# Kernel optimization log

Measured on AMD Instinct MI355X. Metric: run time of the kernel, lower is better.

## Reference

```python
import jax, jax.numpy as jnp
import numpy as np

BATCH = 16384
NUM_IN = 4096
NUM_OUT = 1024
NNZ = 262144
BN_EPS = 1e-3  # keras BatchNormalization default epsilon


def setup_inputs() -> dict:
    key = jax.random.key(0)
    ks = jax.random.split(key, 6)
    x = jax.random.normal(ks[0], (BATCH, NUM_IN), dtype=jnp.float32)
    sp_values = jax.random.normal(ks[1], (NNZ,), dtype=jnp.float32)
    gamma = jnp.ones((NUM_IN,), dtype=jnp.float32)
    beta = jnp.zeros((NUM_IN,), dtype=jnp.float32)
    moving_mean = jax.random.normal(ks[2], (NUM_IN,), dtype=jnp.float32)
    # positive moving variance in [0.5, 1.5)
    moving_var = jax.random.uniform(ks[3], (NUM_IN,), dtype=jnp.float32, minval=0.5, maxval=1.5)
    sp_rows = jax.random.randint(ks[4], (NNZ,), 0, NUM_IN, dtype=jnp.int32)
    sp_cols = jax.random.randint(ks[5], (NNZ,), 0, NUM_OUT, dtype=jnp.int32)
    return {
        "x": x,
        "sp_values": sp_values,
        "gamma": gamma,
        "beta": beta,
        "moving_mean": moving_mean,
        "moving_var": moving_var,
        "sp_rows": sp_rows,
        "sp_cols": sp_cols,
    }


def reference(x, sp_values, gamma, beta, moving_mean, moving_var, sp_rows, sp_cols):
    # BatchNorm (inference mode, moving statistics), fused elementwise
    h = (x - moving_mean) * (gamma * jax.lax.rsqrt(moving_var + BN_EPS)) + beta
    # Scatter the fixed-index sparse weights into a small dense [NUM_IN, NUM_OUT]
    # matrix (16 MB), then a single dense GEMM — honors SparseTensor semantics
    # (duplicate indices accumulate) while staying GEMM-efficient.
    W = jnp.zeros((NUM_IN, NUM_OUT), dtype=x.dtype).at[sp_rows, sp_cols].add(sp_values)
    return h @ W  # [BATCH, NUM_OUT]
```

## Files before the change

### kernel.cpp

```cpp
#include <hip/hip_runtime.h>
#include <hip/hip_bf16.h>

#define BATCH   16384
#define NUM_IN  4096
#define NUM_OUT 1024
#define NNZ     262144
#define BN_EPS  1e-3f

typedef __attribute__((ext_vector_type(8))) short   short8;
typedef __attribute__((ext_vector_type(4))) float   f32x4;
typedef __attribute__((ext_vector_type(4))) unsigned int u32x4;

typedef __attribute__((address_space(3))) void        lds_void_t;
typedef const __attribute__((address_space(1))) void  g_void_t;

__device__ inline unsigned short f2bf(float f) {
    unsigned int u = __builtin_bit_cast(unsigned int, f);
    u += 0x7fffu + ((u >> 16) & 1u);
    return (unsigned short)(u >> 16);
}

__global__ void k_zero(f32x4* __restrict__ p) {
    p[(size_t)blockIdx.x * 256 + threadIdx.x] = f32x4{0.f, 0.f, 0.f, 0.f};
}

__global__ void k_scatter(const float* __restrict__ v, const int* __restrict__ r,
                          const int* __restrict__ c, float* __restrict__ wtf) {
    int i = blockIdx.x * 256 + threadIdx.x;
    atomicAdd(&wtf[(size_t)c[i] * NUM_IN + r[i]], v[i]);
}

__global__ void k_wprep(const float* __restrict__ wtf, const float* __restrict__ gamma,
                        const float* __restrict__ beta, const float* __restrict__ mean,
                        const float* __restrict__ var, unsigned short* __restrict__ wtb,
                        float* __restrict__ bias) {
    const int n = blockIdx.x;
    const int t = threadIdx.x;
    float acc = 0.f;
    for (int k = t; k < NUM_IN; k += 256) {
        float w = wtf[(size_t)n * NUM_IN + k];
        float s = gamma[k] * rsqrtf(var[k] + BN_EPS);
        wtb[(size_t)n * NUM_IN + k] = f2bf(w * s);
        acc += (beta[k] - mean[k] * s) * w;
    }
    #pragma unroll
    for (int o = 32; o; o >>= 1) acc += __shfl_down(acc, o, 64);
    __shared__ float red[4];
    if ((t & 63) == 0) red[t >> 6] = acc;
    __syncthreads();
    if (t == 0) bias[n] = red[0] + red[1] + red[2] + red[3];
}

#define BM 256
#define BN 256
#define BK 32
#define KTILES (NUM_IN / BK)
#define ABYTES 32768
#define BBYTES 16384
#define PBUF   49152

__global__ __launch_bounds__(512, 2) void k_gemm(const float* __restrict__ x,
                                                 const unsigned short* __restrict__ wt,
                                                 const float* __restrict__ bias,
                                                 float* __restrict__ out) {
    __shared__ __align__(128) char lds[3 * PBUF];

    const int bid = blockIdx.x;
    const int swz = (bid & 7) * 32 + (bid >> 3);
    const int m0 = (swz >> 2) * BM;
    const int n0 = (swz & 3) * BN;

    const int t    = threadIdx.x;
    const int lane = t & 63;
    const int wid  = t >> 6;
    const int wm   = wid >> 1;
    const int wn   = wid & 1;

    const char* xb = (const char*)x;
    const char* wb = (const char*)wt;

    const int a_r0 = t >> 3, a_c = (t & 7) * 16;
    const int b_r0 = t >> 2, b_c = (t & 3) * 16;

    auto stage = [&](int kt, int buf) {
        char* base = lds + buf * PBUF;
        #pragma unroll
        for (int q = 0; q < 4; ++q) {
            int row = q * 64 + a_r0;
            size_t src = (size_t)(m0 + row) * (NUM_IN * 4) + kt * (BK * 4)
                       + (a_c ^ ((row & 7) << 4));
            __builtin_amdgcn_global_load_lds((g_void_t*)(xb + src),
                (lds_void_t*)(base + q * 8192 + t * 16), 16, 0, 0);
        }
        #pragma unroll
        for (int q = 0; q < 2; ++q) {
            int row = q * 128 + b_r0;
            size_t src = (size_t)(n0 + row) * (NUM_IN * 2) + kt * (BK * 2)
                       + (b_c ^ (((row >> 1) & 3) << 4));
            __builtin_amdgcn_global_load_lds((g_void_t*)(wb + src),
                (lds_void_t*)(base + ABYTES + q * 8192 + t * 16), 16, 0, 0);
        }
    };

    f32x4 acc[4][8] = {};

    const int a_row0 = wm * 64 + (lane & 15);
    const int a_kb   = (lane >> 4) * 32;
    const int b_row0 = wn * 128 + (lane & 15);
    const int b_kb   = (lane >> 4) * 16;

    auto compute = [&](int buf) {
        const char* A = lds + buf * PBUF;
        const char* B = A + ABYTES;
        short8 bfr[8];
        #pragma unroll
        for (int j = 0; j < 8; ++j) {
            int row = b_row0 + j * 16;
            bfr[j] = *(const short8*)(B + row * 64 + (b_kb ^ (((row >> 1) & 3) << 4)));
        }
        short8 af[4];
        #pragma unroll
        for (int m = 0; m < 4; ++m) {
            int row = a_row0 + m * 16;
            int s = (row & 7) << 4;
            f32x4 lo = *(const f32x4*)(A + row * 128 + (a_kb ^ s));
            f32x4 hi = *(const f32x4*)(A + row * 128 + ((a_kb + 16) ^ s));
            const unsigned int* f0 = (const unsigned int*)&lo;
            const unsigned int* f1 = (const unsigned int*)&hi;
            u32x4 p;
            p[0] = __builtin_amdgcn_perm(f0[1], f0[0], 0x07060302u);
            p[1] = __builtin_amdgcn_perm(f0[3], f0[2], 0x07060302u);
            p[2] = __builtin_amdgcn_perm(f1[1], f1[0], 0x07060302u);
            p[3] = __builtin_amdgcn_perm(f1[3], f1[2], 0x07060302u);
            af[m] = __builtin_bit_cast(short8, p);
        }
        __builtin_amdgcn_s_setprio(1);
        #pragma unroll
        for (int m = 0; m < 4; ++m)
            #pragma unroll
            for (int j = 0; j < 8; ++j)
                acc[m][j] = __builtin_amdgcn_mfma_f32_16x16x32_bf16(af[m], bfr[j],
                                                                    acc[m][j], 0, 0, 0);
        __builtin_amdgcn_s_setprio(0);
    };

    stage(0, 0);
    stage(1, 1);
    asm volatile("s_waitcnt vmcnt(6)" ::: "memory");
    __builtin_amdgcn_s_barrier();
    __builtin_amdgcn_sched_barrier(0);

    int cur = 0, sb = 2;
    for (int kt = 0; kt < KTILES - 2; ++kt) {
        stage(kt + 2, sb);
        compute(cur);
        asm volatile("s_waitcnt vmcnt(6)" ::: "memory");
        __builtin_amdgcn_s_barrier();
        __builtin_amdgcn_sched_barrier(0);
        cur = (cur == 2) ? 0 : cur + 1;
        sb  = (sb  == 2) ? 0 : sb  + 1;
    }
    compute(cur);
    cur = (cur == 2) ? 0 : cur + 1;
    asm volatile("s_waitcnt vmcnt(0)" ::: "memory");
    __builtin_amdgcn_s_barrier();
    __builtin_amdgcn_sched_barrier(0);
    compute(cur);

    float bj[8];
    #pragma unroll
    for (int j = 0; j < 8; ++j) bj[j] = bias[n0 + wn * 128 + j * 16 + (lane & 15)];
    const int mb = m0 + wm * 64 + (lane >> 4) * 4;
    const int nb = n0 + wn * 128 + (lane & 15);
    #pragma unroll
    for (int m = 0; m < 4; ++m)
        #pragma unroll
        for (int j = 0; j < 8; ++j)
            #pragma unroll
            for (int r = 0; r < 4; ++r)
                out[(size_t)(mb + m * 16 + r) * NUM_OUT + (nb + j * 16)] =
                    acc[m][j][r] + bj[j];
}

extern "C" void kernel_launch(void* const* d_in, const int* in_sizes, int n_in,
                              void* d_out, int out_size, void* d_ws, size_t ws_size,
                              hipStream_t stream) {
    const float* x     = (const float*)d_in[0];
    const float* spv   = (const float*)d_in[1];
    const float* gamma = (const float*)d_in[2];
    const float* beta  = (const float*)d_in[3];
    const float* mean  = (const float*)d_in[4];
    const float* var   = (const float*)d_in[5];
    const int*   rows  = (const int*)d_in[6];
    const int*   cols  = (const int*)d_in[7];
    float* out = (float*)d_out;

    float* wtf = (float*)d_out;
    unsigned short* wtb = (unsigned short*)d_ws;
    float* bias = (float*)((char*)d_ws + (size_t)NUM_IN * NUM_OUT * sizeof(unsigned short));

    hipLaunchKernelGGL(k_zero, dim3((NUM_IN * NUM_OUT / 4) / 256), dim3(256), 0, stream,
                       (f32x4*)wtf);
    hipLaunchKernelGGL(k_scatter, dim3(NNZ / 256), dim3(256), 0, stream,
                       spv, rows, cols, wtf);
    hipLaunchKernelGGL(k_wprep, dim3(NUM_OUT), dim3(256), 0, stream,
                       wtf, gamma, beta, mean, var, wtb, bias);
    hipLaunchKernelGGL(k_gemm, dim3((BATCH / BM) * (NUM_OUT / BN)), dim3(512), 0, stream,
                       x, wtb, bias, out);
}
```

Before: 191.1 us.

## Convert A tile to bf16 once in LDS and switch to 32x32x16 MFMA

Result: slower. 238.6 us (+24.9%).

```diff
diff --git a/kernel.cpp b/kernel.cpp
--- a/kernel.cpp
+++ b/kernel.cpp
@@ -7,9 +7,10 @@
 #define NNZ     262144
 #define BN_EPS  1e-3f
 
-typedef __attribute__((ext_vector_type(8))) short   short8;
-typedef __attribute__((ext_vector_type(4))) float   f32x4;
-typedef __attribute__((ext_vector_type(4))) unsigned int u32x4;
+typedef __attribute__((ext_vector_type(8)))  short short8;
+typedef __attribute__((ext_vector_type(4)))  float f32x4;
+typedef __attribute__((ext_vector_type(16))) float f32x16;
+typedef __attribute__((ext_vector_type(4)))  unsigned int u32x4;
 
 typedef __attribute__((address_space(3))) void        lds_void_t;
 typedef const __attribute__((address_space(1))) void  g_void_t;
@@ -54,16 +55,15 @@
 #define BM 256
 #define BN 256
 #define BK 32
-#define KTILES (NUM_IN / BK)
-#define ABYTES 32768
-#define BBYTES 16384
-#define PBUF   49152
+#define NT (NUM_IN / BK)
+#define SLOT 32768
+#define B_OFF 16384
 
 __global__ __launch_bounds__(512, 2) void k_gemm(const float* __restrict__ x,
                                                  const unsigned short* __restrict__ wt,
                                                  const float* __restrict__ bias,
                                                  float* __restrict__ out) {
-    __shared__ __align__(128) char lds[3 * PBUF];
+    __shared__ __align__(128) char lds[4 * SLOT];
 
     const int bid = blockIdx.x;
     const int swz = (bid & 7) * 32 + (bid >> 3);
@@ -73,113 +73,143 @@
     const int t    = threadIdx.x;
     const int lane = t & 63;
     const int wid  = t >> 6;
-    const int wm   = wid >> 1;
-    const int wn   = wid & 1;
+    const int wm   = wid >> 2;
+    const int wn   = wid & 3;
 
     const char* xb = (const char*)x;
     const char* wb = (const char*)wt;
 
-    const int a_r0 = t >> 3, a_c = (t & 7) * 16;
-    const int b_r0 = t >> 2, b_c = (t & 3) * 16;
-
-    auto stage = [&](int kt, int buf) {
-        char* base = lds + buf * PBUF;
-        #pragma unroll
-        for (int q = 0; q < 4; ++q) {
-            int row = q * 64 + a_r0;
-            size_t src = (size_t)(m0 + row) * (NUM_IN * 4) + kt * (BK * 4)
-                       + (a_c ^ ((row & 7) << 4));
-            __builtin_amdgcn_global_load_lds((g_void_t*)(xb + src),
-                (lds_void_t*)(base + q * 8192 + t * 16), 16, 0, 0);
-        }
-        #pragma unroll
-        for (int q = 0; q < 2; ++q) {
-            int row = q * 128 + b_r0;
-            size_t src = (size_t)(n0 + row) * (NUM_IN * 2) + kt * (BK * 2)
-                       + (b_c ^ (((row >> 1) & 3) << 4));
+    const int s_ar  = t >> 1;
+    const int s_ah  = t & 1;
+    const int a_swz = ((s_ar >> 1) & 3) << 4;
+    const int s_bc  = t >> 2;
+    const int s_bk  = (t & 3) * 16;
+
+    f32x4 rA[2][4];
+
+    auto stageB = [&](int kt, int slot) {
+        #pragma unroll
+        for (int i = 0; i < 2; ++i) {
+            int c = i * 128 + s_bc;
+            size_t src = (size_t)(n0 + c) * (NUM_IN * 2) + kt * (BK * 2)
+                       + (s_bk ^ (((c >> 1) & 3) << 4));
             __builtin_amdgcn_global_load_lds((g_void_t*)(wb + src),
-                (lds_void_t*)(base + ABYTES + q * 8192 + t * 16), 16, 0, 0);
-        }
-    };
-
-    f32x4 acc[4][8] = {};
-
-    const int a_row0 = wm * 64 + (lane & 15);
-    const int a_kb   = (lane >> 4) * 32;
-    const int b_row0 = wn * 128 + (lane & 15);
-    const int b_kb   = (lane >> 4) * 16;
-
-    auto compute = [&](int buf) {
-        const char* A = lds + buf * PBUF;
-        const char* B = A + ABYTES;
-        short8 bfr[8];
-        #pragma unroll
-        for (int j = 0; j < 8; ++j) {
-            int row = b_row0 + j * 16;
-            bfr[j] = *(const short8*)(B + row * 64 + (b_kb ^ (((row >> 1) & 3) << 4)));
-        }
-        short8 af[4];
+                (lds_void_t*)(lds + slot * SLOT + B_OFF + i * 8192 + t * 16), 16, 0, 0);
+        }
+    };
+    auto loadA = [&](int kt, int rs) {
+        size_t src = (size_t)(m0 + s_ar) * (NUM_IN * 4) + kt * (BK * 4) + s_ah * 64;
+        #pragma unroll
+        for (int j = 0; j < 4; ++j)
+            rA[rs][j] = *(const f32x4*)(xb + src + j * 16);
+    };
+    auto writeA = [&](int slot, int rs) {
+        const unsigned int* f = (const unsigned int*)&rA[rs][0];
+        u32x4 p0, p1;
+        p0[0] = __builtin_amdgcn_perm(f[1],  f[0],  0x07060302u);
+        p0[1] = __builtin_amdgcn_perm(f[3],  f[2],  0x07060302u);
+        p0[2] = __builtin_amdgcn_perm(f[5],  f[4],  0x07060302u);
+        p0[3] = __builtin_amdgcn_perm(f[7],  f[6],  0x07060302u);
+        p1[0] = __builtin_amdgcn_perm(f[9],  f[8],  0x07060302u);
+        p1[1] = __builtin_amdgcn_perm(f[11], f[10], 0x07060302u);
+        p1[2] = __builtin_amdgcn_perm(f[13], f[12], 0x07060302u);
+        p1[3] = __builtin_amdgcn_perm(f[15], f[14], 0x07060302u);
+        char* dst = lds + slot * SLOT + s_ar * 64;
+        *(u32x4*)(dst + ((s_ah * 32 +  0) ^ a_swz)) = p0;
+        *(u32x4*)(dst + ((s_ah * 32 + 16) ^ a_swz)) = p1;
+    };
+
+    const int fa_row = wm * 128 + (lane & 31);
+    const int fb_col = wn * 64 + (lane & 31);
+    const int f_kb   = (lane >> 5) * 16;
+
+    short8 afr[4], bfr[2];
+    auto readFrags = [&](int slot, int q) {
+        const char* A = lds + slot * SLOT;
+        const char* B = A + B_OFF;
         #pragma unroll
         for (int m = 0; m < 4; ++m) {
-            int row = a_row0 + m * 16;
-            int s = (row & 7) << 4;
-            f32x4 lo = *(const f32x4*)(A + row * 128 + (a_kb ^ s));
-            f32x4 hi = *(const f32x4*)(A + row * 128 + ((a_kb + 16) ^ s));
-            const unsigned int* f0 = (const unsigned int*)&lo;
-            const unsigned int* f1 = (const unsigned int*)&hi;
-            u32x4 p;
-            p[0] = __builtin_amdgcn_perm(f0[1], f0[0], 0x07060302u);
-            p[1] = __builtin_amdgcn_perm(f0[3], f0[2], 0x07060302u);
-            p[2] = __builtin_amdgcn_perm(f1[1], f1[0], 0x07060302u);
-            p[3] = __builtin_amdgcn_perm(f1[3], f1[2], 0x07060302u);
-            af[m] = __builtin_bit_cast(short8, p);
-        }
+            int row = fa_row + m * 32;
+            afr[m] = *(const short8*)(A + row * 64
+                       + ((q * 32 + f_kb) ^ (((row >> 1) & 3) << 4)));
+        }
+        #pragma unroll
+        for (int n = 0; n < 2; ++n) {
+            int col = fb_col + n * 32;
+            bfr[n] = *(const short8*)(B + col * 64
+                       + ((q * 32 + f_kb) ^ (((col >> 1) & 3) << 4)));
+        }
+    };
+
+    f32x16 acc[4][2] = {};
+    auto domfma = [&]() {
         __builtin_amdgcn_s_setprio(1);
         #pragma unroll
         for (int m = 0; m < 4; ++m)
             #pragma unroll
-            for (int j = 0; j < 8; ++j)
-                acc[m][j] = __builtin_amdgcn_mfma_f32_16x16x32_bf16(af[m], bfr[j],
-                                                                    acc[m][j], 0, 0, 0);
+            for (int n = 0; n < 2; ++n)
+                acc[m][n] = __builtin_amdgcn_mfma_f32_32x32x16_bf16(
+                    afr[m], bfr[n], acc[m][n], 0, 0, 0);
         __builtin_amdgcn_s_setprio(0);
     };
 
-    stage(0, 0);
-    stage(1, 1);
+    auto body = [&](int kt, int rs, bool doStage, bool doConv, bool vm0) {
+        const int cs = kt & 3;
+        if (doStage) {
+            stageB(kt + 2, (kt + 2) & 3);
+            loadA(kt + 2, rs);
+            __builtin_amdgcn_sched_barrier(0);
+        }
+        readFrags(cs, 0);
+        asm volatile("s_waitcnt lgkmcnt(0)" ::: "memory");
+        __builtin_amdgcn_sched_barrier(0);
+        domfma();
+        __builtin_amdgcn_s_barrier();
+        readFrags(cs, 1);
+        __builtin_amdgcn_sched_barrier(0);
+        if (doConv) {
+            if (vm0) asm volatile("s_waitcnt vmcnt(0)" ::: "memory");
+            else     asm volatile("s_waitcnt vmcnt(6)" ::: "memory");
+            writeA((kt + 1) & 3, rs ^ 1);
+            asm volatile("s_waitcnt lgkmcnt(2)" ::: "memory");
+        } else {
+            asm volatile("s_waitcnt lgkmcnt(0)" ::: "memory");
+        }
+        __builtin_amdgcn_sched_barrier(0);
+        domfma();
+        asm volatile("s_waitcnt lgkmcnt(0)" ::: "memory");
+        __builtin_amdgcn_s_barrier();
+    };
+
+    stageB(0, 0); loadA(0, 0);
+    stageB(1, 1); loadA(1, 1);
     asm volatile("s_waitcnt vmcnt(6)" ::: "memory");
+    writeA(0, 0);
+    asm volatile("s_waitcnt lgkmcnt(0)" ::: "memory");
     __builtin_amdgcn_s_barrier();
-    __builtin_amdgcn_sched_barrier(0);
-
-    int cur = 0, sb = 2;
-    for (int kt = 0; kt < KTILES - 2; ++kt) {
-        stage(kt + 2, sb);
-        compute(cur);
-        asm volatile("s_waitcnt vmcnt(6)" ::: "memory");
-        __builtin_amdgcn_s_barrier();
-        __builtin_amdgcn_sched_barrier(0);
-        cur = (cur == 2) ? 0 : cur + 1;
-        sb  = (sb  == 2) ? 0 : sb  + 1;
+
+    #pragma unroll 1
+    for (int kt = 0; kt < NT - 2; kt += 2) {
+        body(kt,     0, true, true, false);
+        body(kt + 1, 1, true, true, false);
     }
-    compute(cur);
-    cur = (cur == 2) ? 0 : cur + 1;
-    asm volatile("s_waitcnt vmcnt(0)" ::: "memory");
-    __builtin_amdgcn_s_barrier();
-    __builtin_amdgcn_sched_barrier(0);
-    compute(cur);
-
-    float bj[8];
+    body(NT - 2, 0, false, true, true);
+    body(NT - 1, 1, false, false, false);
+
+    float bj[2];
     #pragma unroll
-    for (int j = 0; j < 8; ++j) bj[j] = bias[n0 + wn * 128 + j * 16 + (lane & 15)];
-    const int mb = m0 + wm * 64 + (lane >> 4) * 4;
-    const int nb = n0 + wn * 128 + (lane & 15);
+    for (int n = 0; n < 2; ++n) bj[n] = bias[n0 + wn * 64 + n * 32 + (lane & 31)];
+    const int rbase = m0 + wm * 128 + 4 * (lane >> 5);
+    const int cbase = n0 + wn * 64 + (lane & 31);
     #pragma unroll
     for (int m = 0; m < 4; ++m)
         #pragma unroll
-        for (int j = 0; j < 8; ++j)
+        for (int n = 0; n < 2; ++n)
             #pragma unroll
-            for (int r = 0; r < 4; ++r)
-                out[(size_t)(mb + m * 16 + r) * NUM_OUT + (nb + j * 16)] =
-                    acc[m][j][r] + bj[j];
+            for (int r = 0; r < 16; ++r) {
+                int row = rbase + m * 32 + (r & 3) + 8 * (r >> 2);
+                out[(size_t)row * NUM_OUT + cbase + n * 32] = acc[m][n][r] + bj[n];
+            }
 }
 
 extern "C" void kernel_launch(void* const* d_in, const int* in_sizes, int n_in,
```

## Split GEMM K-step into two phases interleaving LDS reads, staging and MFMA

Applied to the files above, without the earlier changes.

Measured after the change: 206.3 us. 1.08x slower.

```diff
diff --git a/kernel.cpp b/kernel.cpp
--- a/kernel.cpp
+++ b/kernel.cpp
@@ -7,9 +7,9 @@
 #define NNZ     262144
 #define BN_EPS  1e-3f
 
-typedef __attribute__((ext_vector_type(8))) short   short8;
-typedef __attribute__((ext_vector_type(4))) float   f32x4;
-typedef __attribute__((ext_vector_type(4))) unsigned int u32x4;
+typedef __attribute__((ext_vector_type(8)))  short short8;
+typedef __attribute__((ext_vector_type(4)))  float f32x4;
+typedef __attribute__((ext_vector_type(4)))  unsigned int u32x4;
 
 typedef __attribute__((address_space(3))) void        lds_void_t;
 typedef const __attribute__((address_space(1))) void  g_void_t;
@@ -54,16 +54,16 @@
 #define BM 256
 #define BN 256
 #define BK 32
-#define KTILES (NUM_IN / BK)
-#define ABYTES 32768
-#define BBYTES 16384
-#define PBUF   49152
+#define NT (NUM_IN / BK)
+#define ASLOT 32768
+#define BSLOT 16384
+#define PSLOT 49152
 
 __global__ __launch_bounds__(512, 2) void k_gemm(const float* __restrict__ x,
                                                  const unsigned short* __restrict__ wt,
                                                  const float* __restrict__ bias,
                                                  float* __restrict__ out) {
-    __shared__ __align__(128) char lds[3 * PBUF];
+    __shared__ __align__(128) char lds[3 * PSLOT];
 
     const int bid = blockIdx.x;
     const int swz = (bid & 7) * 32 + (bid >> 3);
@@ -73,60 +73,61 @@
     const int t    = threadIdx.x;
     const int lane = t & 63;
     const int wid  = t >> 6;
-    const int wm   = wid >> 1;
-    const int wn   = wid & 1;
+    const int wm   = wid >> 2;
+    const int wn   = wid & 3;
 
     const char* xb = (const char*)x;
     const char* wb = (const char*)wt;
 
-    const int a_r0 = t >> 3, a_c = (t & 7) * 16;
-    const int b_r0 = t >> 2, b_c = (t & 3) * 16;
-
-    auto stage = [&](int kt, int buf) {
-        char* base = lds + buf * PBUF;
-        #pragma unroll
-        for (int q = 0; q < 4; ++q) {
-            int row = q * 64 + a_r0;
-            size_t src = (size_t)(m0 + row) * (NUM_IN * 4) + kt * (BK * 4)
-                       + (a_c ^ ((row & 7) << 4));
+    auto stageA = [&](int kt, int sl) {
+        #pragma unroll
+        for (int i = 0; i < 4; ++i) {
+            int row = i * 64 + (t >> 3);
+            size_t src = (size_t)(m0 + row) * (NUM_IN * 4) + (size_t)kt * (BK * 4)
+                       + (((t & 7) ^ (row & 7)) * 16);
             __builtin_amdgcn_global_load_lds((g_void_t*)(xb + src),
-                (lds_void_t*)(base + q * 8192 + t * 16), 16, 0, 0);
-        }
-        #pragma unroll
-        for (int q = 0; q < 2; ++q) {
-            int row = q * 128 + b_r0;
-            size_t src = (size_t)(n0 + row) * (NUM_IN * 2) + kt * (BK * 2)
-                       + (b_c ^ (((row >> 1) & 3) << 4));
+                (lds_void_t*)(lds + sl * PSLOT + i * 8192 + t * 16), 16, 0, 0);
+        }
+    };
+    auto stageB = [&](int kt, int sl) {
+        #pragma unroll
+        for (int i = 0; i < 2; ++i) {
+            int row = i * 128 + (t >> 2);
+            size_t src = (size_t)(n0 + row) * (NUM_IN * 2) + (size_t)kt * (BK * 2)
+                       + (((t & 3) ^ ((row >> 1) & 3)) * 16);
             __builtin_amdgcn_global_load_lds((g_void_t*)(wb + src),
-                (lds_void_t*)(base + ABYTES + q * 8192 + t * 16), 16, 0, 0);
-        }
-    };
-
-    f32x4 acc[4][8] = {};
-
-    const int a_row0 = wm * 64 + (lane & 15);
-    const int a_kb   = (lane >> 4) * 32;
-    const int b_row0 = wn * 128 + (lane & 15);
-    const int b_kb   = (lane >> 4) * 16;
-
-    auto compute = [&](int buf) {
-        const char* A = lds + buf * PBUF;
-        const char* B = A + ABYTES;
-        short8 bfr[8];
-        #pragma unroll
-        for (int j = 0; j < 8; ++j) {
-            int row = b_row0 + j * 16;
-            bfr[j] = *(const short8*)(B + row * 64 + (b_kb ^ (((row >> 1) & 3) << 4)));
-        }
-        short8 af[4];
+                (lds_void_t*)(lds + sl * PSLOT + ASLOT + i * 8192 + t * 16), 16, 0, 0);
+        }
+    };
+
+    const int fr   = lane & 15;
+    const int a_k0 = (lane >> 4) * 32;
+    const int b_k0 = (lane >> 4) * 16;
+
+    f32x4 alo[4], ahi[4];
+    short8 af[4], bfr[4];
+
+    auto readB4 = [&](const char* B) {
+        #pragma unroll
+        for (int n = 0; n < 4; ++n) {
+            int row = wn * 64 + n * 16 + fr;
+            bfr[n] = *(const short8*)(B + row * 64 + (b_k0 ^ (((row >> 1) & 3) << 4)));
+        }
+    };
+    auto readA4 = [&](const char* A, int mh) {
         #pragma unroll
         for (int m = 0; m < 4; ++m) {
-            int row = a_row0 + m * 16;
+            int row = wm * 128 + (mh + m) * 16 + fr;
             int s = (row & 7) << 4;
-            f32x4 lo = *(const f32x4*)(A + row * 128 + (a_kb ^ s));
-            f32x4 hi = *(const f32x4*)(A + row * 128 + ((a_kb + 16) ^ s));
-            const unsigned int* f0 = (const unsigned int*)&lo;
-            const unsigned int* f1 = (const unsigned int*)&hi;
+            alo[m] = *(const f32x4*)(A + row * 128 + (a_k0 ^ s));
+            ahi[m] = *(const f32x4*)(A + row * 128 + ((a_k0 + 16) ^ s));
+        }
+    };
+    auto convA = [&]() {
+        #pragma unroll
+        for (int m = 0; m < 4; ++m) {
+            const unsigned int* f0 = (const unsigned int*)&alo[m];
+            const unsigned int* f1 = (const unsigned int*)&ahi[m];
             u32x4 p;
             p[0] = __builtin_amdgcn_perm(f0[1], f0[0], 0x07060302u);
             p[1] = __builtin_amdgcn_perm(f0[3], f0[2], 0x07060302u);
@@ -134,52 +135,67 @@
             p[3] = __builtin_amdgcn_perm(f1[3], f1[2], 0x07060302u);
             af[m] = __builtin_bit_cast(short8, p);
         }
+    };
+
+    f32x4 acc[8][4] = {};
+    auto mfma16 = [&](int mh) {
         __builtin_amdgcn_s_setprio(1);
         #pragma unroll
         for (int m = 0; m < 4; ++m)
             #pragma unroll
-            for (int j = 0; j < 8; ++j)
-                acc[m][j] = __builtin_amdgcn_mfma_f32_16x16x32_bf16(af[m], bfr[j],
-                                                                    acc[m][j], 0, 0, 0);
+            for (int n = 0; n < 4; ++n)
+                acc[mh + m][n] = __builtin_amdgcn_mfma_f32_16x16x32_bf16(
+                    af[m], bfr[n], acc[mh + m][n], 0, 0, 0);
         __builtin_amdgcn_s_setprio(0);
     };
 
-    stage(0, 0);
-    stage(1, 1);
+    stageA(0, 0); stageB(0, 0);
+    stageA(1, 1); stageB(1, 1);
     asm volatile("s_waitcnt vmcnt(6)" ::: "memory");
     __builtin_amdgcn_s_barrier();
-    __builtin_amdgcn_sched_barrier(0);
-
-    int cur = 0, sb = 2;
-    for (int kt = 0; kt < KTILES - 2; ++kt) {
-        stage(kt + 2, sb);
-        compute(cur);
-        asm volatile("s_waitcnt vmcnt(6)" ::: "memory");
-        __builtin_amdgcn_s_barrier();
+
+    int cur = 0;
+    #pragma unroll 1
+    for (int kt = 0; kt < NT; ++kt) {
+        const bool st = (kt + 2) < NT;
+        const int stg = (cur >= 1) ? cur - 1 : cur + 2;
+        const char* A = lds + cur * PSLOT;
+        const char* B = A + ASLOT;
+        if (st) stageA(kt + 2, stg);
+        readB4(B);
+        readA4(A, 0);
+        __builtin_amdgcn_s_barrier();
+        asm volatile("s_waitcnt lgkmcnt(0)" ::: "memory");
         __builtin_amdgcn_sched_barrier(0);
-        cur = (cur == 2) ? 0 : cur + 1;
-        sb  = (sb  == 2) ? 0 : sb  + 1;
+        convA();
+        mfma16(0);
+        __builtin_amdgcn_s_barrier();
+        if (st) stageB(kt + 2, stg);
+        readA4(A, 4);
+        if (st) asm volatile("s_waitcnt vmcnt(6)" ::: "memory");
+        else    asm volatile("s_waitcnt vmcnt(0)" ::: "memory");
+        __builtin_amdgcn_s_barrier();
+        asm volatile("s_waitcnt lgkmcnt(0)" ::: "memory");
+        __builtin_amdgcn_sched_barrier(0);
+        convA();
+        mfma16(4);
+        __builtin_amdgcn_s_barrier();
+        cur = (cur < 2) ? cur + 1 : 0;
     }
-    compute(cur);
-    cur = (cur == 2) ? 0 : cur + 1;
-    asm volatile("s_waitcnt vmcnt(0)" ::: "memory");
-    __builtin_amdgcn_s_barrier();
-    __builtin_amdgcn_sched_barrier(0);
-    compute(cur);
-
-    float bj[8];
+
+    float bj[4];
     #pragma unroll
-    for (int j = 0; j < 8; ++j) bj[j] = bias[n0 + wn * 128 + j * 16 + (lane & 15)];
-    const int mb = m0 + wm * 64 + (lane >> 4) * 4;
-    const int nb = n0 + wn * 128 + (lane & 15);
+    for (int n = 0; n < 4; ++n) bj[n] = bias[n0 + wn * 64 + n * 16 + fr];
+    const int mb = m0 + wm * 128 + (lane >> 4) * 4;
+    const int nb = n0 + wn * 64 + fr;
     #pragma unroll
-    for (int m = 0; m < 4; ++m)
-        #pragma unroll
-        for (int j = 0; j < 8; ++j)
+    for (int m = 0; m < 8; ++m)
+        #pragma unroll
+        for (int n = 0; n < 4; ++n)
             #pragma unroll
             for (int r = 0; r < 4; ++r)
-                out[(size_t)(mb + m * 16 + r) * NUM_OUT + (nb + j * 16)] =
-                    acc[m][j][r] + bj[j];
+                out[(size_t)(mb + m * 16 + r) * NUM_OUT + (nb + n * 16)] =
+                    acc[m][n][r] + bj[n];
 }
 
 extern "C" void kernel_launch(void* const* d_in, const int* in_sizes, int n_in,
```
